# Performance work log

Measured on AMD Instinct MI355X. Metric: run time of the kernel, lower is better.

The kernel has to match this reference:

```python
import jax, jax.numpy as jnp
import numpy as np

B, N, D = 4, 2048, 1024  # in_features == out_features required by the original code path
SPARSITY = 0.01


def setup_inputs() -> dict:
    key = jax.random.key(0)
    k1, k2, k3 = jax.random.split(key, 3)
    x = jax.random.normal(k1, (B, N, D), dtype=jnp.float32)
    # Reproduce FrequencyLinearLayer.__init__: sparse top-k frequency weights.
    spatial = jax.random.normal(k2, (D, D), dtype=jnp.float32) * 0.02
    freq = jnp.fft.fft(spatial, axis=-1)  # complex64, (out, in) consumed as (D_in, D_out)
    k = int(D * SPARSITY)
    mag = jnp.abs(freq)
    kth = jax.lax.top_k(mag, k)[0][:, -1:]  # k-th largest magnitude per row
    w_sparse = jnp.where(mag >= kth, freq, 0.0 + 0.0j)
    bias = jax.random.normal(k3, (D,), dtype=jnp.float32) * 0.01
    return {
        "x": x,
        "w_freq_real": jnp.real(w_sparse).astype(jnp.float32),
        "w_freq_imag": jnp.imag(w_sparse).astype(jnp.float32),
        "bias": bias,
    }


def reference(x, w_freq_real, w_freq_imag, bias):
    # y = real(IFFT(FFT(x) @ W_freq)) + bias
    # The original materializes a (B,N,D_in,D_out) complex intermediate via
    # unsqueeze*multiply -> sum; that is exactly a complex matmul, expressed here as einsum.
    w = jax.lax.complex(w_freq_real, w_freq_imag)            # (D_in, D_out) complex64
    x_freq = jnp.fft.fft(x, axis=-1)                          # (B, N, D_in) complex64
    y_freq = jnp.einsum('bnd,do->bno', x_freq, w)             # (B, N, D_out)
    y = jnp.real(jnp.fft.ifft(y_freq, axis=-1))               # (B, N, D_out) float32
    return y + bias
```

## Files before the change

kernel.cpp:

```cpp
#include <hip/hip_runtime.h>
#include <hip/hip_bf16.h>
#include <math.h>

#define DD 1024
#define BT 8192
#define TWO_PI 6.28318530717958647692f

typedef float f32x4 __attribute__((ext_vector_type(4)));
typedef short bf16x8 __attribute__((ext_vector_type(8)));
typedef unsigned short u16x8 __attribute__((ext_vector_type(8)));
typedef unsigned short u16x4 __attribute__((ext_vector_type(4)));
typedef const __attribute__((address_space(1))) void g_void;
typedef __attribute__((address_space(3))) void l_void;

__device__ __forceinline__ unsigned short f2bf(float f) {
  unsigned int u = __float_as_uint(f);
  unsigned int r = (u + 0x7FFFu + ((u >> 16) & 1u)) >> 16;
  return (unsigned short)r;
}

__global__ __launch_bounds__(256) void transpose_W_kernel(
    const float* __restrict__ Wr, const float* __restrict__ Wi,
    float2* __restrict__ Wt) {
  __shared__ float tr[64][65];
  __shared__ float ti[64][65];
  const int k0 = blockIdx.y * 64, o0 = blockIdx.x * 64;
  for (int q = threadIdx.x; q < 64 * 64; q += 256) {
    int r = q >> 6, c = q & 63;
    tr[r][c] = Wr[(size_t)(k0 + r) * DD + o0 + c];
    ti[r][c] = Wi[(size_t)(k0 + r) * DD + o0 + c];
  }
  __syncthreads();
  for (int q = threadIdx.x; q < 64 * 64; q += 256) {
    int r = q >> 6, c = q & 63;
    Wt[(size_t)(o0 + r) * DD + k0 + c] = make_float2(tr[c][r], ti[c][r]);
  }
}

__global__ __launch_bounds__(256) void build_T_kernel(
    const float2* __restrict__ Wt, float2* __restrict__ T) {
  __shared__ float2 tw[DD];
  __shared__ int    kidx[64];
  __shared__ float2 wval[64];
  __shared__ int    sc[256];
  const int o = blockIdx.x, tid = threadIdx.x;

  for (int j = tid; j < DD; j += 256) {
    float s, c;
    sincosf((TWO_PI / DD) * (float)j, &s, &c);
    tw[j] = make_float2(c, s);
  }
  int cnt = 0;
  float2 wl[4];
  int    kl[4];
#pragma unroll
  for (int q = 0; q < 4; q++) {
    int k = tid + q * 256;
    float2 w = Wt[(size_t)o * DD + k];
    if (w.x != 0.f || w.y != 0.f) { wl[cnt] = w; kl[cnt] = k; cnt++; }
  }
  sc[tid] = cnt;
  __syncthreads();
#pragma unroll
  for (int dstep = 1; dstep < 256; dstep <<= 1) {
    int v = (tid >= dstep) ? sc[tid - dstep] : 0;
    __syncthreads();
    sc[tid] += v;
    __syncthreads();
  }
  int p = sc[tid] - cnt;
  for (int q = 0; q < cnt; q++) { kidx[p + q] = kl[q]; wval[p + q] = wl[q]; }
  __syncthreads();
  const int nnz = sc[255];
  for (int d = tid; d < DD; d += 256) {
    float re = 0.f, im = 0.f;
    for (int j = 0; j < nnz; j++) {
      int    k  = kidx[j];
      float2 w  = wval[j];
      float2 cs = tw[(k * d) & (DD - 1)];
      re += w.x * cs.x + w.y * cs.y;
      im += w.y * cs.x - w.x * cs.y;
    }
    T[(size_t)o * DD + d] = make_float2(re, im);
  }
}

__global__ __launch_bounds__(256) void transpose_T_kernel(
    const float2* __restrict__ T, unsigned short* __restrict__ TT) {
  __shared__ float2 tile[64][65];
  const int o0 = blockIdx.x * 64, d0 = blockIdx.y * 64;
  for (int q = threadIdx.x; q < 64 * 64; q += 256) {
    int r = q >> 6, c = q & 63;
    tile[r][c] = T[(size_t)(o0 + r) * DD + d0 + c];
  }
  __syncthreads();
  for (int q = threadIdx.x; q < 64 * 64; q += 256) {
    int r = q >> 6, c = q & 63;
    float2 v = tile[c][r];
    TT[(size_t)(d0 + r) * 2048 + o0 + c]        = f2bf(v.x);
    TT[(size_t)(d0 + r) * 2048 + 1024 + o0 + c] = f2bf(v.y);
  }
}

__global__ __launch_bounds__(256) void convert_x_kernel(
    const float* __restrict__ X, unsigned short* __restrict__ Xb) {
  size_t i = (size_t)blockIdx.x * 256 + threadIdx.x;
  const float4* p = (const float4*)(X + i * 8);
  float4 a = p[0], b = p[1];
  u16x8 v;
  v[0] = f2bf(a.x); v[1] = f2bf(a.y); v[2] = f2bf(a.z); v[3] = f2bf(a.w);
  v[4] = f2bf(b.x); v[5] = f2bf(b.y); v[6] = f2bf(b.z); v[7] = f2bf(b.w);
  *(u16x8*)(Xb + i * 8) = v;
}

__global__ __launch_bounds__(256) void build_M_kernel(
    const unsigned short* __restrict__ B,
    float* __restrict__ P, int kLen) {
  __shared__ __align__(16) unsigned short Asm[128 * 32];
  __shared__ __align__(16) unsigned short Bsm[128 * 32];
  const int tid  = threadIdx.x;
  const int wave = tid >> 6, lane = tid & 63;
  const int wr = wave >> 1, wc = wave & 1;
  const int row0 = blockIdx.y * 128;
  const int col0 = blockIdx.x * 128;
  const int kBeg = blockIdx.z * kLen;

  f32x4 acc[4][4] = {};

  for (int k0 = kBeg; k0 < kBeg + kLen; k0 += 32) {
    __syncthreads();
#pragma unroll
    for (int is = 0; is < 2; is++) {
      int e = is * 256 + tid;
      int r = e >> 2, c = (e & 3) * 8;
      const unsigned short* gb = B + (size_t)(col0 + r) * 2048 + k0 + c;
      __builtin_amdgcn_global_load_lds((g_void*)gb,
          (l_void*)(Bsm + is * 2048 + wave * 512), 16, 0, 0);
    }
#pragma unroll
    for (int is = 0; is < 2; is++) {
      int e = is * 256 + tid;
      int r = e >> 2, c = (e & 3) * 8;
      int m = row0 + r;
      u16x8 v;
#pragma unroll
      for (int q = 0; q < 8; q++) {
        int kg   = k0 + c + q;
        int o    = kg & (DD - 1);
        int idx  = (m * o) & (DD - 1);
        float s, cc;
        __sincosf((TWO_PI / DD) * (float)idx, &s, &cc);
        v[q] = f2bf((kg < DD) ? cc : -s);
      }
      *(u16x8*)(Asm + e * 8) = v;
    }
    __syncthreads();

    bf16x8 af[4], bfr[4];
#pragma unroll
    for (int i = 0; i < 4; i++) {
      int ra = wr * 64 + i * 16 + (lane & 15);
      af[i]  = *(const bf16x8*)&Asm[ra * 32 + (lane >> 4) * 8];
      int rb = wc * 64 + i * 16 + (lane & 15);
      bfr[i] = *(const bf16x8*)&Bsm[rb * 32 + (lane >> 4) * 8];
    }
#pragma unroll
    for (int i = 0; i < 4; i++)
#pragma unroll
      for (int j = 0; j < 4; j++)
        acc[i][j] = __builtin_amdgcn_mfma_f32_16x16x32_bf16(af[i], bfr[j], acc[i][j], 0, 0, 0);
  }

  const int crow0 = row0 + wr * 64;
  const int ccol0 = col0 + wc * 64;
  float* O = P + (size_t)blockIdx.z * DD * DD;
#pragma unroll
  for (int i = 0; i < 4; i++)
#pragma unroll
    for (int j = 0; j < 4; j++) {
      int cc = ccol0 + j * 16 + (lane & 15);
#pragma unroll
      for (int v = 0; v < 4; v++) {
        int rr = crow0 + i * 16 + (lane >> 4) * 4 + v;
        O[(size_t)rr * DD + cc] = acc[i][j][v];
      }
    }
}

template <int NZ>
__global__ __launch_bounds__(256) void reduce_M_kernel(
    const float* __restrict__ P, unsigned short* __restrict__ Mb) {
  const size_t NE = (size_t)DD * DD;
  size_t i = ((size_t)blockIdx.x * 256 + threadIdx.x) * 4;
  float4 s = *(const float4*)(P + i);
#pragma unroll
  for (int z = 1; z < NZ; z++) {
    float4 p = *(const float4*)(P + z * NE + i);
    s.x += p.x; s.y += p.y; s.z += p.z; s.w += p.w;
  }
  const float inv = 1.0f / (float)DD;
  u16x4 v;
  v[0] = f2bf(s.x * inv); v[1] = f2bf(s.y * inv);
  v[2] = f2bf(s.z * inv); v[3] = f2bf(s.w * inv);
  *(u16x4*)(Mb + i) = v;
}

__global__ __launch_bounds__(512) void gemm_y_kernel(
    const unsigned short* __restrict__ Xb,
    const unsigned short* __restrict__ Mb,
    const float* __restrict__ bias,
    float* __restrict__ Y) {
  __shared__ __align__(16) unsigned short Asm[2][128 * 32];
  __shared__ __align__(16) unsigned short Bsm[2][128 * 32];
  const int tid  = threadIdx.x;
  const int wave = tid >> 6, lane = tid & 63;
  const int kw   = wave >> 2;
  const int w4   = wave & 3;
  const int wr   = w4 >> 1, wc = w4 & 1;
  const int t256 = tid & 255;
  const int row0 = blockIdx.y * 128;
  const int col0 = blockIdx.x * 128;
  const int kBeg = kw * 512;

  f32x4 acc[4][4] = {};

  for (int k0 = kBeg; k0 < kBeg + 512; k0 += 32) {
    __syncthreads();
#pragma unroll
    for (int is = 0; is < 2; is++) {
      int e = is * 256 + t256;
      int r = e >> 2, c = (e & 3) * 8;
      const unsigned short* ga = Xb + (size_t)(row0 + r) * DD + k0 + c;
      const unsigned short* gb = Mb + (size_t)(col0 + r) * DD + k0 + c;
      __builtin_amdgcn_global_load_lds((g_void*)ga,
          (l_void*)(Asm[kw] + is * 2048 + w4 * 512), 16, 0, 0);
      __builtin_amdgcn_global_load_lds((g_void*)gb,
          (l_void*)(Bsm[kw] + is * 2048 + w4 * 512), 16, 0, 0);
    }
    __syncthreads();

    bf16x8 af[4], bfr[4];
#pragma unroll
    for (int i = 0; i < 4; i++) {
      int ra = wr * 64 + i * 16 + (lane & 15);
      af[i]  = *(const bf16x8*)&Asm[kw][ra * 32 + (lane >> 4) * 8];
      int rb = wc * 64 + i * 16 + (lane & 15);
      bfr[i] = *(const bf16x8*)&Bsm[kw][rb * 32 + (lane >> 4) * 8];
    }
#pragma unroll
    for (int i = 0; i < 4; i++)
#pragma unroll
      for (int j = 0; j < 4; j++)
        acc[i][j] = __builtin_amdgcn_mfma_f32_16x16x32_bf16(af[i], bfr[j], acc[i][j], 0, 0, 0);
  }

  const int crow0 = row0 + wr * 64;
  const int ccol0 = col0 + wc * 64;
  float bv[4];
#pragma unroll
  for (int j = 0; j < 4; j++)
    bv[j] = bias[ccol0 + j * 16 + (lane & 15)];

  float* red = (float*)Asm;
#pragma unroll
  for (int i = 0; i < 4; i++) {
    __syncthreads();
    if (kw == 1) {
      float* dst = red + (w4 * 64 + lane) * 16;
#pragma unroll
      for (int j = 0; j < 4; j++) *(f32x4*)(dst + j * 4) = acc[i][j];
    }
    __syncthreads();
    if (kw == 0) {
      const float* src = red + (w4 * 64 + lane) * 16;
#pragma unroll
      for (int j = 0; j < 4; j++) {
        f32x4 oth = *(const f32x4*)(src + j * 4);
        int cc = ccol0 + j * 16 + (lane & 15);
#pragma unroll
        for (int v = 0; v < 4; v++) {
          int rr = crow0 + i * 16 + (lane >> 4) * 4 + v;
          Y[(size_t)rr * DD + cc] = acc[i][j][v] + oth[v] + bv[j];
        }
      }
    }
  }
}

extern "C" void kernel_launch(void* const* d_in, const int* in_sizes, int n_in,
                              void* d_out, int out_size, void* d_ws, size_t ws_size,
                              hipStream_t stream) {
  const float* x    = (const float*)d_in[0];
  const float* wrp  = (const float*)d_in[1];
  const float* wip  = (const float*)d_in[2];
  const float* bias = (const float*)d_in[3];
  float*       y    = (float*)d_out;

  char* ws = (char*)d_ws;
  const size_t MB = 1024 * 1024;
  float2*         Wt = (float2*)(ws + 0);
  float2*         T  = (float2*)(ws + 8  * MB);
  unsigned short* TT = (unsigned short*)(ws + 16 * MB);
  unsigned short* Mb = (unsigned short*)(ws + 24 * MB);
  float*          P  = (float*)(ws + 32 * MB);
  unsigned short* Xb = (unsigned short*)(ws + 0);

  transpose_W_kernel<<<dim3(16, 16), 256, 0, stream>>>(wrp, wip, Wt);
  build_T_kernel<<<DD, 256, 0, stream>>>(Wt, T);
  transpose_T_kernel<<<dim3(16, 16), 256, 0, stream>>>(T, TT);
  build_M_kernel<<<dim3(8, 8, 4), 256, 0, stream>>>(TT, P, 512);
  reduce_M_kernel<4><<<DD * DD / (256 * 4), 256, 0, stream>>>(P, Mb);
  convert_x_kernel<<<4096, 256, 0, stream>>>(x, Xb);
  gemm_y_kernel<<<dim3(8, 64), 512, 0, stream>>>(Xb, Mb, bias, y);
}
```

Baseline: 103.8 us.

## Replace split-K GEMM with triple-buffered pipelined single-K loop and swizzled LDS

```diff
diff --git a/kernel.cpp b/kernel.cpp
--- a/kernel.cpp
+++ b/kernel.cpp
@@ -205,54 +205,75 @@
   *(u16x4*)(Mb + i) = v;
 }
 
-__global__ __launch_bounds__(512) void gemm_y_kernel(
+__global__ __launch_bounds__(256) void gemm_y_kernel(
     const unsigned short* __restrict__ Xb,
     const unsigned short* __restrict__ Mb,
     const float* __restrict__ bias,
     float* __restrict__ Y) {
-  __shared__ __align__(16) unsigned short Asm[2][128 * 32];
-  __shared__ __align__(16) unsigned short Bsm[2][128 * 32];
+  __shared__ __align__(16) unsigned short Asm[3][128 * 32];
+  __shared__ __align__(16) unsigned short Bsm[3][128 * 32];
   const int tid  = threadIdx.x;
   const int wave = tid >> 6, lane = tid & 63;
-  const int kw   = wave >> 2;
-  const int w4   = wave & 3;
-  const int wr   = w4 >> 1, wc = w4 & 1;
-  const int t256 = tid & 255;
+  const int wr = wave >> 1, wc = wave & 1;
   const int row0 = blockIdx.y * 128;
   const int col0 = blockIdx.x * 128;
-  const int kBeg = kw * 512;
+  const int NT = DD / 32;
+
+#define STAGE_Y(buf, kk)                                                     \
+  {                                                                          \
+    _Pragma("unroll")                                                        \
+    for (int is = 0; is < 2; is++) {                                         \
+      int e  = is * 256 + tid;                                               \
+      int r  = e >> 2;                                                       \
+      int cb = ((e & 3) ^ ((e >> 3) & 3)) * 8;   \
+      const unsigned short* ga = Xb + (size_t)(row0 + r) * DD + (kk) + cb;   \
+      const unsigned short* gb = Mb + (size_t)(col0 + r) * DD + (kk) + cb;   \
+      __builtin_amdgcn_global_load_lds((g_void*)ga,                          \
+          (l_void*)(Asm[buf] + is * 2048 + wave * 512), 16, 0, 0);           \
+      __builtin_amdgcn_global_load_lds((g_void*)gb,                          \
+          (l_void*)(Bsm[buf] + is * 2048 + wave * 512), 16, 0, 0);           \
+    }                                                                        \
+  }
 
   f32x4 acc[4][4] = {};
 
-  for (int k0 = kBeg; k0 < kBeg + 512; k0 += 32) {
-    __syncthreads();
-#pragma unroll
-    for (int is = 0; is < 2; is++) {
-      int e = is * 256 + t256;
-      int r = e >> 2, c = (e & 3) * 8;
-      const unsigned short* ga = Xb + (size_t)(row0 + r) * DD + k0 + c;
-      const unsigned short* gb = Mb + (size_t)(col0 + r) * DD + k0 + c;
-      __builtin_amdgcn_global_load_lds((g_void*)ga,
-          (l_void*)(Asm[kw] + is * 2048 + w4 * 512), 16, 0, 0);
-      __builtin_amdgcn_global_load_lds((g_void*)gb,
-          (l_void*)(Bsm[kw] + is * 2048 + w4 * 512), 16, 0, 0);
-    }
-    __syncthreads();
+  STAGE_Y(0, 0);
+  STAGE_Y(1, 32);
+
+  int cur = 0;
+  for (int t = 0; t < NT; ++t) {
+    if (t < NT - 1) {
+      asm volatile("s_waitcnt vmcnt(4)" ::: "memory");
+    } else {
+      asm volatile("s_waitcnt vmcnt(0)" ::: "memory");
+    }
+    __builtin_amdgcn_s_barrier();
+    __builtin_amdgcn_sched_barrier(0);
+
+    if (t < NT - 2) {
+      int nb = cur + 2; if (nb >= 3) nb -= 3;
+      STAGE_Y(nb, (t + 2) * 32);
+    }
 
     bf16x8 af[4], bfr[4];
 #pragma unroll
     for (int i = 0; i < 4; i++) {
       int ra = wr * 64 + i * 16 + (lane & 15);
-      af[i]  = *(const bf16x8*)&Asm[kw][ra * 32 + (lane >> 4) * 8];
+      int ca = ((lane >> 4) ^ ((ra >> 1) & 3)) * 8;
+      af[i]  = *(const bf16x8*)&Asm[cur][ra * 32 + ca];
       int rb = wc * 64 + i * 16 + (lane & 15);
-      bfr[i] = *(const bf16x8*)&Bsm[kw][rb * 32 + (lane >> 4) * 8];
+      int cb = ((lane >> 4) ^ ((rb >> 1) & 3)) * 8;
+      bfr[i] = *(const bf16x8*)&Bsm[cur][rb * 32 + cb];
     }
 #pragma unroll
     for (int i = 0; i < 4; i++)
 #pragma unroll
       for (int j = 0; j < 4; j++)
         acc[i][j] = __builtin_amdgcn_mfma_f32_16x16x32_bf16(af[i], bfr[j], acc[i][j], 0, 0, 0);
-  }
+
+    cur = cur + 1 == 3 ? 0 : cur + 1;
+  }
+#undef STAGE_Y
 
   const int crow0 = row0 + wr * 64;
   const int ccol0 = col0 + wc * 64;
@@ -260,31 +281,17 @@
 #pragma unroll
   for (int j = 0; j < 4; j++)
     bv[j] = bias[ccol0 + j * 16 + (lane & 15)];
-
-  float* red = (float*)Asm;
-#pragma unroll
-  for (int i = 0; i < 4; i++) {
-    __syncthreads();
-    if (kw == 1) {
-      float* dst = red + (w4 * 64 + lane) * 16;
-#pragma unroll
-      for (int j = 0; j < 4; j++) *(f32x4*)(dst + j * 4) = acc[i][j];
-    }
-    __syncthreads();
-    if (kw == 0) {
-      const float* src = red + (w4 * 64 + lane) * 16;
-#pragma unroll
-      for (int j = 0; j < 4; j++) {
-        f32x4 oth = *(const f32x4*)(src + j * 4);
-        int cc = ccol0 + j * 16 + (lane & 15);
-#pragma unroll
-        for (int v = 0; v < 4; v++) {
-          int rr = crow0 + i * 16 + (lane >> 4) * 4 + v;
-          Y[(size_t)rr * DD + cc] = acc[i][j][v] + oth[v] + bv[j];
-        }
+#pragma unroll
+  for (int i = 0; i < 4; i++)
+#pragma unroll
+    for (int j = 0; j < 4; j++) {
+      int cc = ccol0 + j * 16 + (lane & 15);
+#pragma unroll
+      for (int v = 0; v < 4; v++) {
+        int rr = crow0 + i * 16 + (lane >> 4) * 4 + v;
+        Y[(size_t)rr * DD + cc] = acc[i][j][v] + bv[j];
       }
     }
-  }
 }
 
 extern "C" void kernel_launch(void* const* d_in, const int* in_sizes, int n_in,
@@ -311,5 +318,5 @@
   build_M_kernel<<<dim3(8, 8, 4), 256, 0, stream>>>(TT, P, 512);
   reduce_M_kernel<4><<<DD * DD / (256 * 4), 256, 0, stream>>>(P, Mb);
   convert_x_kernel<<<4096, 256, 0, stream>>>(x, Xb);
-  gemm_y_kernel<<<dim3(8, 64), 512, 0, stream>>>(Xb, Mb, bias, y);
-}
+  gemm_y_kernel<<<dim3(8, 64), 256, 0, stream>>>(Xb, Mb, bias, y);
+}
```

Result: no change. 102.6 us (-1.1%).

## Rebuild weight-matrix precompute as fused sparse G-kernel and merge small passes

Applied to the files above, without the earlier changes.

```diff
diff --git a/kernel.cpp b/kernel.cpp
--- a/kernel.cpp
+++ b/kernel.cpp
@@ -19,102 +19,76 @@
   return (unsigned short)r;
 }
 
-__global__ __launch_bounds__(256) void transpose_W_kernel(
+__global__ __launch_bounds__(256) void build_G_kernel(
     const float* __restrict__ Wr, const float* __restrict__ Wi,
-    float2* __restrict__ Wt) {
-  __shared__ float tr[64][65];
-  __shared__ float ti[64][65];
-  const int k0 = blockIdx.y * 64, o0 = blockIdx.x * 64;
-  for (int q = threadIdx.x; q < 64 * 64; q += 256) {
-    int r = q >> 6, c = q & 63;
-    tr[r][c] = Wr[(size_t)(k0 + r) * DD + o0 + c];
-    ti[r][c] = Wi[(size_t)(k0 + r) * DD + o0 + c];
-  }
-  __syncthreads();
-  for (int q = threadIdx.x; q < 64 * 64; q += 256) {
-    int r = q >> 6, c = q & 63;
-    Wt[(size_t)(o0 + r) * DD + k0 + c] = make_float2(tr[c][r], ti[c][r]);
-  }
-}
-
-__global__ __launch_bounds__(256) void build_T_kernel(
-    const float2* __restrict__ Wt, float2* __restrict__ T) {
+    unsigned short* __restrict__ Gt) {
   __shared__ float2 tw[DD];
-  __shared__ int    kidx[64];
-  __shared__ float2 wval[64];
-  __shared__ int    sc[256];
-  const int o = blockIdx.x, tid = threadIdx.x;
+  __shared__ int    cntA[64];
+  __shared__ int    oA[64][24];
+  __shared__ float  wrA[64][24];
+  __shared__ float  wiA[64][24];
+  const int tid = threadIdx.x, wave = tid >> 6, lane = tid & 63;
+  const int mt = blockIdx.x;
+  const int ks = blockIdx.y;
+  const int kbase = ks * 64;
 
   for (int j = tid; j < DD; j += 256) {
     float s, c;
     sincosf((TWO_PI / DD) * (float)j, &s, &c);
     tw[j] = make_float2(c, s);
   }
-  int cnt = 0;
-  float2 wl[4];
-  int    kl[4];
-#pragma unroll
-  for (int q = 0; q < 4; q++) {
-    int k = tid + q * 256;
-    float2 w = Wt[(size_t)o * DD + k];
-    if (w.x != 0.f || w.y != 0.f) { wl[cnt] = w; kl[cnt] = k; cnt++; }
-  }
-  sc[tid] = cnt;
+  for (int rr = 0; rr < 16; ++rr) {
+    int kl = wave * 16 + rr;
+    int k  = kbase + kl;
+    int cnt = 0;
+    for (int cc = 0; cc < 16; ++cc) {
+      int o = cc * 64 + lane;
+      float wr = Wr[(size_t)k * DD + o];
+      float wi = Wi[(size_t)k * DD + o];
+      bool nz = (wr != 0.f) || (wi != 0.f);
+      unsigned long long mk = __ballot(nz);
+      if (nz) {
+        int pos = cnt + (int)__popcll(mk & ((1ull << lane) - 1ull));
+        if (pos < 24) { oA[kl][pos] = o; wrA[kl][pos] = wr; wiA[kl][pos] = wi; }
+      }
+      cnt += (int)__popcll(mk);
+    }
+    if (lane == 0) cntA[kl] = cnt > 24 ? 24 : cnt;
+  }
   __syncthreads();
-#pragma unroll
-  for (int dstep = 1; dstep < 256; dstep <<= 1) {
-    int v = (tid >= dstep) ? sc[tid - dstep] : 0;
-    __syncthreads();
-    sc[tid] += v;
-    __syncthreads();
-  }
-  int p = sc[tid] - cnt;
-  for (int q = 0; q < cnt; q++) { kidx[p + q] = kl[q]; wval[p + q] = wl[q]; }
-  __syncthreads();
-  const int nnz = sc[255];
-  for (int d = tid; d < DD; d += 256) {
-    float re = 0.f, im = 0.f;
-    for (int j = 0; j < nnz; j++) {
-      int    k  = kidx[j];
-      float2 w  = wval[j];
-      float2 cs = tw[(k * d) & (DD - 1)];
-      re += w.x * cs.x + w.y * cs.y;
-      im += w.y * cs.x - w.x * cs.y;
-    }
-    T[(size_t)o * DD + d] = make_float2(re, im);
-  }
-}
-
-__global__ __launch_bounds__(256) void transpose_T_kernel(
-    const float2* __restrict__ T, unsigned short* __restrict__ TT) {
-  __shared__ float2 tile[64][65];
-  const int o0 = blockIdx.x * 64, d0 = blockIdx.y * 64;
-  for (int q = threadIdx.x; q < 64 * 64; q += 256) {
-    int r = q >> 6, c = q & 63;
-    tile[r][c] = T[(size_t)(o0 + r) * DD + d0 + c];
-  }
-  __syncthreads();
-  for (int q = threadIdx.x; q < 64 * 64; q += 256) {
-    int r = q >> 6, c = q & 63;
-    float2 v = tile[c][r];
-    TT[(size_t)(d0 + r) * 2048 + o0 + c]        = f2bf(v.x);
-    TT[(size_t)(d0 + r) * 2048 + 1024 + o0 + c] = f2bf(v.y);
-  }
-}
-
-__global__ __launch_bounds__(256) void convert_x_kernel(
-    const float* __restrict__ X, unsigned short* __restrict__ Xb) {
-  size_t i = (size_t)blockIdx.x * 256 + threadIdx.x;
-  const float4* p = (const float4*)(X + i * 8);
-  float4 a = p[0], b = p[1];
-  u16x8 v;
-  v[0] = f2bf(a.x); v[1] = f2bf(a.y); v[2] = f2bf(a.z); v[3] = f2bf(a.w);
-  v[4] = f2bf(b.x); v[5] = f2bf(b.y); v[6] = f2bf(b.z); v[7] = f2bf(b.w);
-  *(u16x8*)(Xb + i * 8) = v;
+
+  const int ml = tid >> 1;
+  const int kh = tid & 1;
+  const int m  = mt * 128 + ml;
+  float gre[32], gim[32];
+#pragma unroll
+  for (int q = 0; q < 32; q++) { gre[q] = 0.f; gim[q] = 0.f; }
+#pragma unroll
+  for (int q = 0; q < 32; q++) {
+    int kl = kh * 32 + q;
+    int n  = cntA[kl];
+    for (int j = 0; j < n; ++j) {
+      int   o  = oA[kl][j];
+      float wr = wrA[kl][j];
+      float wi = wiA[kl][j];
+      float2 cs = tw[(m * o) & (DD - 1)];
+      gre[q] += wr * cs.x - wi * cs.y;
+      gim[q] += wr * cs.y + wi * cs.x;
+    }
+  }
+  size_t base = (size_t)m * 2048 + kbase + kh * 32;
+#pragma unroll
+  for (int v = 0; v < 4; v++) {
+    u16x8 a, b;
+#pragma unroll
+    for (int q = 0; q < 8; q++) { a[q] = f2bf(gre[v * 8 + q]); b[q] = f2bf(gim[v * 8 + q]); }
+    *(u16x8*)(Gt + base + v * 8)        = a;
+    *(u16x8*)(Gt + base + 1024 + v * 8) = b;
+  }
 }
 
 __global__ __launch_bounds__(256) void build_M_kernel(
-    const unsigned short* __restrict__ B,
+    const unsigned short* __restrict__ Gt,
     float* __restrict__ P, int kLen) {
   __shared__ __align__(16) unsigned short Asm[128 * 32];
   __shared__ __align__(16) unsigned short Bsm[128 * 32];
@@ -133,26 +107,25 @@
     for (int is = 0; is < 2; is++) {
       int e = is * 256 + tid;
       int r = e >> 2, c = (e & 3) * 8;
-      const unsigned short* gb = B + (size_t)(col0 + r) * 2048 + k0 + c;
-      __builtin_amdgcn_global_load_lds((g_void*)gb,
-          (l_void*)(Bsm + is * 2048 + wave * 512), 16, 0, 0);
+      const unsigned short* ga = Gt + (size_t)(row0 + r) * 2048 + k0 + c;
+      __builtin_amdgcn_global_load_lds((g_void*)ga,
+          (l_void*)(Asm + is * 2048 + wave * 512), 16, 0, 0);
     }
 #pragma unroll
     for (int is = 0; is < 2; is++) {
       int e = is * 256 + tid;
       int r = e >> 2, c = (e & 3) * 8;
-      int m = row0 + r;
+      int d = col0 + r;
       u16x8 v;
 #pragma unroll
       for (int q = 0; q < 8; q++) {
-        int kg   = k0 + c + q;
-        int o    = kg & (DD - 1);
-        int idx  = (m * o) & (DD - 1);
+        int K   = k0 + c + q;
+        int idx = (K * d) & (DD - 1);
         float s, cc;
         __sincosf((TWO_PI / DD) * (float)idx, &s, &cc);
-        v[q] = f2bf((kg < DD) ? cc : -s);
-      }
-      *(u16x8*)(Asm + e * 8) = v;
+        v[q] = f2bf((K < DD) ? cc : s);
+      }
+      *(u16x8*)(Bsm + e * 8) = v;
     }
     __syncthreads();
 
@@ -187,55 +160,62 @@
     }
 }
 
-template <int NZ>
-__global__ __launch_bounds__(256) void reduce_M_kernel(
-    const float* __restrict__ P, unsigned short* __restrict__ Mb) {
-  const size_t NE = (size_t)DD * DD;
-  size_t i = ((size_t)blockIdx.x * 256 + threadIdx.x) * 4;
-  float4 s = *(const float4*)(P + i);
-#pragma unroll
-  for (int z = 1; z < NZ; z++) {
-    float4 p = *(const float4*)(P + z * NE + i);
-    s.x += p.x; s.y += p.y; s.z += p.z; s.w += p.w;
-  }
-  const float inv = 1.0f / (float)DD;
-  u16x4 v;
-  v[0] = f2bf(s.x * inv); v[1] = f2bf(s.y * inv);
-  v[2] = f2bf(s.z * inv); v[3] = f2bf(s.w * inv);
-  *(u16x4*)(Mb + i) = v;
-}
-
-__global__ __launch_bounds__(512) void gemm_y_kernel(
+__global__ __launch_bounds__(256) void reduce_convert_kernel(
+    const float* __restrict__ P, unsigned short* __restrict__ Mb,
+    const float* __restrict__ X, unsigned short* __restrict__ Xb) {
+  const int b = blockIdx.x;
+  if (b < 1024) {
+    const size_t NE = (size_t)DD * DD;
+    size_t i = ((size_t)b * 256 + threadIdx.x) * 4;
+    float4 s = *(const float4*)(P + i);
+#pragma unroll
+    for (int z = 1; z < 4; z++) {
+      float4 p = *(const float4*)(P + z * NE + i);
+      s.x += p.x; s.y += p.y; s.z += p.z; s.w += p.w;
+    }
+    const float inv = 1.0f / (float)DD;
+    u16x4 v;
+    v[0] = f2bf(s.x * inv); v[1] = f2bf(s.y * inv);
+    v[2] = f2bf(s.z * inv); v[3] = f2bf(s.w * inv);
+    *(u16x4*)(Mb + i) = v;
+  } else {
+    size_t i = (size_t)(b - 1024) * 256 + threadIdx.x;
+    const float4* p = (const float4*)(X + i * 8);
+    float4 a = p[0], c = p[1];
+    u16x8 v;
+    v[0] = f2bf(a.x); v[1] = f2bf(a.y); v[2] = f2bf(a.z); v[3] = f2bf(a.w);
+    v[4] = f2bf(c.x); v[5] = f2bf(c.y); v[6] = f2bf(c.z); v[7] = f2bf(c.w);
+    *(u16x8*)(Xb + i * 8) = v;
+  }
+}
+
+__global__ __launch_bounds__(256) void gemm_y_kernel(
     const unsigned short* __restrict__ Xb,
     const unsigned short* __restrict__ Mb,
     const float* __restrict__ bias,
     float* __restrict__ Y) {
-  __shared__ __align__(16) unsigned short Asm[2][128 * 32];
-  __shared__ __align__(16) unsigned short Bsm[2][128 * 32];
+  __shared__ __align__(16) unsigned short Asm[128 * 32];
+  __shared__ __align__(16) unsigned short Bsm[128 * 32];
   const int tid  = threadIdx.x;
   const int wave = tid >> 6, lane = tid & 63;
-  const int kw   = wave >> 2;
-  const int w4   = wave & 3;
-  const int wr   = w4 >> 1, wc = w4 & 1;
-  const int t256 = tid & 255;
+  const int wr = wave >> 1, wc = wave & 1;
   const int row0 = blockIdx.y * 128;
   const int col0 = blockIdx.x * 128;
-  const int kBeg = kw * 512;
 
   f32x4 acc[4][4] = {};
 
-  for (int k0 = kBeg; k0 < kBeg + 512; k0 += 32) {
+  for (int k0 = 0; k0 < DD; k0 += 32) {
     __syncthreads();
 #pragma unroll
     for (int is = 0; is < 2; is++) {
-      int e = is * 256 + t256;
+      int e = is * 256 + tid;
       int r = e >> 2, c = (e & 3) * 8;
       const unsigned short* ga = Xb + (size_t)(row0 + r) * DD + k0 + c;
       const unsigned short* gb = Mb + (size_t)(col0 + r) * DD + k0 + c;
       __builtin_amdgcn_global_load_lds((g_void*)ga,
-          (l_void*)(Asm[kw] + is * 2048 + w4 * 512), 16, 0, 0);
+          (l_void*)(Asm + is * 2048 + wave * 512), 16, 0, 0);
       __builtin_amdgcn_global_load_lds((g_void*)gb,
-          (l_void*)(Bsm[kw] + is * 2048 + w4 * 512), 16, 0, 0);
+          (l_void*)(Bsm + is * 2048 + wave * 512), 16, 0, 0);
     }
     __syncthreads();
 
@@ -243,9 +223,9 @@
 #pragma unroll
     for (int i = 0; i < 4; i++) {
       int ra = wr * 64 + i * 16 + (lane & 15);
-      af[i]  = *(const bf16x8*)&Asm[kw][ra * 32 + (lane >> 4) * 8];
+      af[i]  = *(const bf16x8*)&Asm[ra * 32 + (lane >> 4) * 8];
       int rb = wc * 64 + i * 16 + (lane & 15);
-      bfr[i] = *(const bf16x8*)&Bsm[kw][rb * 32 + (lane >> 4) * 8];
+      bfr[i] = *(const bf16x8*)&Bsm[rb * 32 + (lane >> 4) * 8];
     }
 #pragma unroll
     for (int i = 0; i < 4; i++)
@@ -260,31 +240,17 @@
 #pragma unroll
   for (int j = 0; j < 4; j++)
     bv[j] = bias[ccol0 + j * 16 + (lane & 15)];
-
-  float* red = (float*)Asm;
-#pragma unroll
-  for (int i = 0; i < 4; i++) {
-    __syncthreads();
-    if (kw == 1) {
-      float* dst = red + (w4 * 64 + lane) * 16;
-#pragma unroll
-      for (int j = 0; j < 4; j++) *(f32x4*)(dst + j * 4) = acc[i][j];
-    }
-    __syncthreads();
-    if (kw == 0) {
-      const float* src = red + (w4 * 64 + lane) * 16;
-#pragma unroll
-      for (int j = 0; j < 4; j++) {
-        f32x4 oth = *(const f32x4*)(src + j * 4);
-        int cc = ccol0 + j * 16 + (lane & 15);
-#pragma unroll
-        for (int v = 0; v < 4; v++) {
-          int rr = crow0 + i * 16 + (lane >> 4) * 4 + v;
-          Y[(size_t)rr * DD + cc] = acc[i][j][v] + oth[v] + bv[j];
-        }
-      }
-    }
-  }
+#pragma unroll
+  for (int i = 0; i < 4; i++)
+#pragma unroll
+    for (int j = 0; j < 4; j++) {
+      int cc = ccol0 + j * 16 + (lane & 15);
+#pragma unroll
+      for (int v = 0; v < 4; v++) {
+        int rr = crow0 + i * 16 + (lane >> 4) * 4 + v;
+        Y[(size_t)rr * DD + cc] = acc[i][j][v] + bv[j];
+      }
+    }
 }
 
 extern "C" void kernel_launch(void* const* d_in, const int* in_sizes, int n_in,
@@ -298,18 +264,13 @@
 
   char* ws = (char*)d_ws;
   const size_t MB = 1024 * 1024;
-  float2*         Wt = (float2*)(ws + 0);
-  float2*         T  = (float2*)(ws + 8  * MB);
-  unsigned short* TT = (unsigned short*)(ws + 16 * MB);
-  unsigned short* Mb = (unsigned short*)(ws + 24 * MB);
-  float*          P  = (float*)(ws + 32 * MB);
-  unsigned short* Xb = (unsigned short*)(ws + 0);
-
-  transpose_W_kernel<<<dim3(16, 16), 256, 0, stream>>>(wrp, wip, Wt);
-  build_T_kernel<<<DD, 256, 0, stream>>>(Wt, T);
-  transpose_T_kernel<<<dim3(16, 16), 256, 0, stream>>>(T, TT);
-  build_M_kernel<<<dim3(8, 8, 4), 256, 0, stream>>>(TT, P, 512);
-  reduce_M_kernel<4><<<DD * DD / (256 * 4), 256, 0, stream>>>(P, Mb);
-  convert_x_kernel<<<4096, 256, 0, stream>>>(x, Xb);
-  gemm_y_kernel<<<dim3(8, 64), 512, 0, stream>>>(Xb, Mb, bias, y);
-}
+  unsigned short* Gt = (unsigned short*)(ws + 0);
+  unsigned short* Mb = (unsigned short*)(ws + 4 * MB);
+  float*          P  = (float*)(ws + 16 * MB);
+  unsigned short* Xb = (unsigned short*)(ws + 32 * MB);
+
+  build_G_kernel<<<dim3(8, 16), 256, 0, stream>>>(wrp, wip, Gt);
+  build_M_kernel<<<dim3(8, 8, 4), 256, 0, stream>>>(Gt, P, 512);
+  reduce_convert_kernel<<<5120, 256, 0, stream>>>(P, Mb, x, Xb);
+  gemm_y_kernel<<<dim3(8, 64), 256, 0, stream>>>(Xb, Mb, bias, y);
+}
```

Result: slower. 161.5 us (+55.7%).
